# Kernel tuning notes

Hardware: AMD Instinct MI355X
Metric: run time of the kernel (lower is better)

The kernel has to match this reference:

```python
import jax, jax.numpy as jnp
import numpy as np

# Jamba mamba mixer dims
H = 4096      # hidden_size
D = 8192      # intermediate_size = mamba_expand * hidden_size
N = 16        # ssm_state_size (mamba_d_state)
K = 4         # conv_kernel_size (mamba_d_conv)
R = 256       # time_step_rank (mamba_dt_rank)
BATCH = 1
L = 2048
EPS = 1e-6


def setup_inputs() -> dict:
    key = jax.random.key(0)
    ks = jax.random.split(key, 10)
    s = 0.02
    return {
        "hidden_states": jax.random.normal(ks[0], (BATCH, L, H), jnp.float32),
        "W_in": jax.random.normal(ks[1], (2 * D, H), jnp.float32) * s,
        "conv_w": jax.random.normal(ks[2], (D, K), jnp.float32) * s,
        "conv_b": jax.random.normal(ks[3], (D,), jnp.float32) * s,
        "Wx": jax.random.normal(ks[4], (R + 2 * N, D), jnp.float32) * s,
        "dt_ln_w": jnp.ones((R,), jnp.float32),
        "b_ln_w": jnp.ones((N,), jnp.float32),
        "c_ln_w": jnp.ones((N,), jnp.float32),
        "Wdt": jax.random.normal(ks[5], (D, R), jnp.float32) * s,
        "dt_bias": jax.random.normal(ks[6], (D,), jnp.float32) * s,
        "A": -jnp.exp(jax.random.normal(ks[7], (D, N), jnp.float32) * 0.5),  # A = -exp(A_log)
        "D_param": jnp.ones((D,), jnp.float32),
        "W_out": jax.random.normal(ks[8], (H, D), jnp.float32) * s,
    }


def _rmsnorm(x, w):
    return x * jax.lax.rsqrt(jnp.mean(x * x, axis=-1, keepdims=True) + EPS) * w


def reference(hidden_states, W_in, conv_w, conv_b, Wx, dt_ln_w, b_ln_w, c_ln_w,
              Wdt, dt_bias, A, D_param, W_out):
    # in_proj -> [B, L, 2D]; split into ssm branch and gate
    proj = hidden_states @ W_in.T
    u, gate = jnp.split(proj, 2, axis=-1)

    # causal depthwise conv1d over sequence dim, then SiLU (causal_conv1d_fn)
    x = jnp.transpose(u, (0, 2, 1))  # [B, D, L]
    x = jax.lax.conv_general_dilated(
        x, conv_w[:, None, :], window_strides=(1,), padding=[(K - 1, 0)],
        dimension_numbers=("NCH", "OIH", "NCH"), feature_group_count=D)
    u = jax.nn.silu(jnp.transpose(x, (0, 2, 1)) + conv_b)  # [B, L, D]

    # x_proj -> dt / B / C with RMSNorms
    ssm_p = u @ Wx.T  # [B, L, R + 2N]
    dt, Bm, Cm = jnp.split(ssm_p, [R, R + N], axis=-1)
    dt = _rmsnorm(dt, dt_ln_w)
    Bm = _rmsnorm(Bm, b_ln_w)
    Cm = _rmsnorm(Cm, c_ln_w)

    # dt_proj (skip_bias_add: bias folded into softplus, delta_softplus=True)
    delta = jax.nn.softplus(dt @ Wdt.T + dt_bias)  # [B, L, D]

    # selective scan: state [B, D, N], recurrence over L
    def step(state, xs):
        d_t, B_t, C_t, u_t = xs  # [B,D], [B,N], [B,N], [B,D]
        dA = jnp.exp(d_t[..., None] * A)                       # [B, D, N]
        state = dA * state + (d_t * u_t)[..., None] * B_t[:, None, :]
        y_t = jnp.einsum("bdn,bn->bd", state, C_t)
        return state, y_t

    init = jnp.zeros((hidden_states.shape[0], D, N), hidden_states.dtype)
    xs = (jnp.swapaxes(delta, 0, 1), jnp.swapaxes(Bm, 0, 1),
          jnp.swapaxes(Cm, 0, 1), jnp.swapaxes(u, 0, 1))
    _, ys = jax.lax.scan(step, init, xs)  # ys: [L, B, D]

    y = jnp.swapaxes(ys, 0, 1) + u * D_param   # skip connection u * D
    y = y * jax.nn.silu(gate)                  # gated output
    return y @ W_out.T                         # out_proj -> [B, L, H]
```

## Files before the change

kernel.cpp:

```cpp
#include <hip/hip_runtime.h>
#include <stdint.h>


#define LSEQ 2048
#define HDIM 4096
#define DDIM 8192
#define NST  16
#define NPAD 384
#define NC   16
#define CLEN 128

typedef __bf16 bf16x8 __attribute__((ext_vector_type(8)));
typedef float  f32x4  __attribute__((ext_vector_type(4)));

__device__ __forceinline__ ushort f2b(float f) {
  uint32_t x = __float_as_uint(f);
  x += 0x7FFFu + ((x >> 16) & 1u);
  return (ushort)(x >> 16);
}
__device__ __forceinline__ float b2f(ushort u) {
  return __uint_as_float(((uint32_t)u) << 16);
}

__device__ __forceinline__ void gload_lds16(const ushort* g, ushort* l) {
  __builtin_amdgcn_global_load_lds(
      (const __attribute__((address_space(1))) void*)g,
      (__attribute__((address_space(3))) void*)l, 16, 0, 0);
}

__global__ __launch_bounds__(256) void cvt_kernel(const float* __restrict__ s,
                                                  ushort* __restrict__ d,
                                                  size_t n8) {
  size_t i = (size_t)blockIdx.x * 256 + threadIdx.x;
  if (i >= n8) return;
  const float4* sp = (const float4*)s;
  float4 a = sp[2 * i], b = sp[2 * i + 1];
  union { ushort us[8]; uint4 v; } u;
  u.us[0] = f2b(a.x); u.us[1] = f2b(a.y); u.us[2] = f2b(a.z); u.us[3] = f2b(a.w);
  u.us[4] = f2b(b.x); u.us[5] = f2b(b.y); u.us[6] = f2b(b.z); u.us[7] = f2b(b.w);
  ((uint4*)d)[i] = u.v;
}

template <int EPI>
__global__ __launch_bounds__(256) void gemm_nt(
    const ushort* __restrict__ A, const ushort* __restrict__ Bw,
    float* __restrict__ C, int M, int N, int ldk, int Kc,
    const float* __restrict__ bias) {
  __shared__ __align__(16) ushort As[128 * 64];
  __shared__ __align__(16) ushort Bs[128 * 64];
  const int tid  = threadIdx.x;
  const int lane = tid & 63;
  const int wid  = tid >> 6;
  const int wr = wid >> 1, wc = wid & 1;
  const int m0 = blockIdx.y * 128, n0 = blockIdx.x * 128;
  const int kbeg = blockIdx.z * Kc;
  C += (size_t)blockIdx.z * M * N;
  const int rr0 = tid >> 3;
  const int sl  = tid & 7;
  const int lrow = lane & 15;
  const int lks  = lane >> 4;

  f32x4 acc[4][4] = {};

  for (int k0 = kbeg; k0 < kbeg + Kc; k0 += 64) {
#pragma unroll
    for (int i = 0; i < 4; ++i) {
      int rr  = i * 32 + rr0;
      int ksl = sl ^ (rr & 7);
      const ushort* ga = A  + (size_t)(m0 + rr) * ldk + k0 + ksl * 8;
      const ushort* gb = Bw + (size_t)(n0 + rr) * ldk + k0 + ksl * 8;
      ushort* la = As + (i * 256 + (wid << 6)) * 8;
      ushort* lb = Bs + (i * 256 + (wid << 6)) * 8;
      gload_lds16(ga, la);
      gload_lds16(gb, lb);
    }
    __syncthreads();
#pragma unroll
    for (int kc = 0; kc < 2; ++kc) {
      bf16x8 av[4], bv[4];
#pragma unroll
      for (int mi = 0; mi < 4; ++mi) {
        int row = wr * 64 + mi * 16 + lrow;
        int ks  = kc * 4 + lks;
        av[mi] = *(const bf16x8*)(As + row * 64 + ((ks ^ (row & 7)) << 3));
      }
#pragma unroll
      for (int ni = 0; ni < 4; ++ni) {
        int row = wc * 64 + ni * 16 + lrow;
        int ks  = kc * 4 + lks;
        bv[ni] = *(const bf16x8*)(Bs + row * 64 + ((ks ^ (row & 7)) << 3));
      }
#pragma unroll
      for (int mi = 0; mi < 4; ++mi)
#pragma unroll
        for (int ni = 0; ni < 4; ++ni)
          acc[mi][ni] = __builtin_amdgcn_mfma_f32_16x16x32_bf16(
              av[mi], bv[ni], acc[mi][ni], 0, 0, 0);
    }
    __syncthreads();
  }

#pragma unroll
  for (int mi = 0; mi < 4; ++mi) {
    int row0 = m0 + wr * 64 + mi * 16 + (lks << 2);
#pragma unroll
    for (int ni = 0; ni < 4; ++ni) {
      int col = n0 + wc * 64 + ni * 16 + lrow;
      float bcol = 0.f;
      if (EPI == 1) bcol = bias[col];
#pragma unroll
      for (int q = 0; q < 4; ++q) {
        float v = acc[mi][ni][q];
        if (EPI == 1) {
          v += bcol;
          v = (v > 20.f) ? v : log1pf(__expf(v));
        }
        C[(size_t)(row0 + q) * N + col] = v;
      }
    }
  }
}

__global__ __launch_bounds__(256) void reduce8_kernel(
    const float* __restrict__ Cp, float* __restrict__ out) {
  size_t i = (size_t)blockIdx.x * 256 + threadIdx.x;
  const size_t MN = (size_t)LSEQ * NPAD;
  float s = 0.f;
#pragma unroll
  for (int z = 0; z < 8; ++z) s += Cp[z * MN + i];
  out[i] = s;
}

__global__ __launch_bounds__(256) void conv_silu_kernel(
    const float* __restrict__ ubuf, const float* __restrict__ cw,
    const float* __restrict__ cb, ushort* __restrict__ uc) {
  int d = blockIdx.x * 256 + threadIdx.x;
  int l = blockIdx.y;
  float4 w4 = ((const float4*)cw)[d];
  float wa[4] = {w4.x, w4.y, w4.z, w4.w};
  float s = cb[d];
#pragma unroll
  for (int j = 0; j < 4; ++j) {
    int li = l - 3 + j;
    if (li >= 0) s += wa[j] * ubuf[(size_t)li * DDIM + d];
  }
  float o = s / (1.f + __expf(-s));
  uc[(size_t)l * DDIM + d] = f2b(o);
}

__global__ __launch_bounds__(64) void norms_kernel(
    const float* __restrict__ ssmp, const float* __restrict__ dtw,
    const float* __restrict__ bw, const float* __restrict__ cwn,
    ushort* __restrict__ dtn, float* __restrict__ Bn, float* __restrict__ Cn) {
  int l = blockIdx.x, lane = threadIdx.x;
  const float* row = ssmp + (size_t)l * NPAD;
  float4 v = ((const float4*)row)[lane];
  float va[4] = {v.x, v.y, v.z, v.w};
  float ss = va[0]*va[0] + va[1]*va[1] + va[2]*va[2] + va[3]*va[3];
#pragma unroll
  for (int m = 32; m >= 1; m >>= 1) ss += __shfl_xor(ss, m);
  float rs = rsqrtf(ss * (1.f / 256.f) + 1e-6f);
  float4 w = ((const float4*)dtw)[lane];
  float wa[4] = {w.x, w.y, w.z, w.w};
  union { ushort us[4]; uint2 v2; } o;
#pragma unroll
  for (int j = 0; j < 4; ++j) o.us[j] = f2b(va[j] * rs * wa[j]);
  ((uint2*)(dtn + (size_t)l * 256))[lane] = o.v2;

  int g = lane & 15;
  float bv = row[256 + g], cv = row[272 + g];
  float bs = bv * bv, cs = cv * cv;
#pragma unroll
  for (int m = 8; m >= 1; m >>= 1) {
    bs += __shfl_xor(bs, m);
    cs += __shfl_xor(cs, m);
  }
  if (lane < 16) {
    Bn[(size_t)l * NST + lane] = bv * rsqrtf(bs * (1.f / 16.f) + 1e-6f) * bw[lane];
    Cn[(size_t)l * NST + lane] = cv * rsqrtf(cs * (1.f / 16.f) + 1e-6f) * cwn[lane];
  }
}


__global__ __launch_bounds__(256) void scan_phase1(
    const float* __restrict__ delta, const ushort* __restrict__ uc,
    const float* __restrict__ Bn, const float* __restrict__ Am,
    float* __restrict__ Sbuf, float* __restrict__ Pbuf) {
  __shared__ float sB[CLEN * NST];
  const int tid = threadIdx.x;
  const int d = blockIdx.x * 256 + tid;
  const int c = blockIdx.y, l0 = c * CLEN;
  {
    const float4* bsrc = (const float4*)(Bn + (size_t)l0 * NST);
    float4* bdst = (float4*)sB;
    for (int i = tid; i < CLEN * NST / 4; i += 256) bdst[i] = bsrc[i];
  }
  __syncthreads();
  float A[16];
#pragma unroll
  for (int j = 0; j < 4; ++j) {
    float4 a4 = ((const float4*)(Am + (size_t)d * NST))[j];
    A[4*j] = a4.x; A[4*j+1] = a4.y; A[4*j+2] = a4.z; A[4*j+3] = a4.w;
  }
  float st[16] = {};
  float sd = 0.f;
  const size_t base = (size_t)l0 * DDIM + d;
  float dx0 = delta[base],            dx1 = delta[base + DDIM];
  float ux0 = b2f(uc[base]),          ux1 = b2f(uc[base + DDIM]);
  for (int l = 0; l < CLEN; l += 2) {
    int lp = (l + 2 < CLEN) ? l + 2 : CLEN - 2;
    float dxn0 = delta[base + (size_t)lp * DDIM];
    float dxn1 = delta[base + (size_t)(lp + 1) * DDIM];
    float uxn0 = b2f(uc[base + (size_t)lp * DDIM]);
    float uxn1 = b2f(uc[base + (size_t)(lp + 1) * DDIM]);
    sd += dx0;
    float dxu = dx0 * ux0;
#pragma unroll
    for (int n = 0; n < 16; ++n)
      st[n] = fmaf(__expf(dx0 * A[n]), st[n], dxu * sB[l * NST + n]);
    sd += dx1;
    dxu = dx1 * ux1;
#pragma unroll
    for (int n = 0; n < 16; ++n)
      st[n] = fmaf(__expf(dx1 * A[n]), st[n], dxu * sB[(l + 1) * NST + n]);
    dx0 = dxn0; dx1 = dxn1; ux0 = uxn0; ux1 = uxn1;
  }
  float4* Sd = (float4*)(Sbuf + ((size_t)c * DDIM + d) * NST);
  float4* Pd = (float4*)(Pbuf + ((size_t)c * DDIM + d) * NST);
#pragma unroll
  for (int j = 0; j < 4; ++j) {
    Sd[j] = make_float4(st[4*j], st[4*j+1], st[4*j+2], st[4*j+3]);
    Pd[j] = make_float4(__expf(A[4*j] * sd),   __expf(A[4*j+1] * sd),
                        __expf(A[4*j+2] * sd), __expf(A[4*j+3] * sd));
  }
}

__global__ __launch_bounds__(256) void scan_phase2(
    const float* __restrict__ Sbuf, float* __restrict__ Pbuf) {
  size_t t = (size_t)blockIdx.x * 256 + threadIdx.x;
  const size_t stride = (size_t)DDIM * NST;
  float s = 0.f;
  for (int c = 0; c < NC; ++c) {
    float P = Pbuf[c * stride + t];
    float S = Sbuf[c * stride + t];
    Pbuf[c * stride + t] = s;
    s = fmaf(P, s, S);
  }
}

__global__ __launch_bounds__(256) void scan_phase3(
    const float* __restrict__ delta, const ushort* __restrict__ uc,
    const float* __restrict__ Bn, const float* __restrict__ Cn,
    const float* __restrict__ Am, const float* __restrict__ Ibuf,
    const float* __restrict__ gbuf, const float* __restrict__ Dp,
    ushort* __restrict__ yg) {
  __shared__ float sB[CLEN * NST];
  __shared__ float sC[CLEN * NST];
  const int tid = threadIdx.x;
  const int d = blockIdx.x * 256 + tid;
  const int c = blockIdx.y, l0 = c * CLEN;
  {
    const float4* bsrc = (const float4*)(Bn + (size_t)l0 * NST);
    const float4* csrc = (const float4*)(Cn + (size_t)l0 * NST);
    float4* bdst = (float4*)sB;
    float4* cdst = (float4*)sC;
    for (int i = tid; i < CLEN * NST / 4; i += 256) {
      bdst[i] = bsrc[i];
      cdst[i] = csrc[i];
    }
  }
  __syncthreads();
  float A[16], st[16];
#pragma unroll
  for (int j = 0; j < 4; ++j) {
    float4 a4 = ((const float4*)(Am + (size_t)d * NST))[j];
    A[4*j] = a4.x; A[4*j+1] = a4.y; A[4*j+2] = a4.z; A[4*j+3] = a4.w;
    float4 s4 = ((const float4*)(Ibuf + ((size_t)c * DDIM + d) * NST))[j];
    st[4*j] = s4.x; st[4*j+1] = s4.y; st[4*j+2] = s4.z; st[4*j+3] = s4.w;
  }
  const float Dpd = Dp[d];
  const size_t base = (size_t)l0 * DDIM + d;
  float dx0 = delta[base],   dx1 = delta[base + DDIM];
  float ux0 = b2f(uc[base]), ux1 = b2f(uc[base + DDIM]);
  float g0  = gbuf[base],    g1  = gbuf[base + DDIM];
  for (int l = 0; l < CLEN; l += 2) {
    int lp = (l + 2 < CLEN) ? l + 2 : CLEN - 2;
    float dxn0 = delta[base + (size_t)lp * DDIM];
    float dxn1 = delta[base + (size_t)(lp + 1) * DDIM];
    float uxn0 = b2f(uc[base + (size_t)lp * DDIM]);
    float uxn1 = b2f(uc[base + (size_t)(lp + 1) * DDIM]);
    float gn0  = gbuf[base + (size_t)lp * DDIM];
    float gn1  = gbuf[base + (size_t)(lp + 1) * DDIM];
    {
      float dxu = dx0 * ux0, y0 = 0.f, y1 = 0.f;
#pragma unroll
      for (int n = 0; n < 16; n += 2) {
        st[n]   = fmaf(__expf(dx0 * A[n]),   st[n],   dxu * sB[l * NST + n]);
        st[n+1] = fmaf(__expf(dx0 * A[n+1]), st[n+1], dxu * sB[l * NST + n+1]);
        y0 = fmaf(st[n],   sC[l * NST + n],   y0);
        y1 = fmaf(st[n+1], sC[l * NST + n+1], y1);
      }
      float o = (y0 + y1 + ux0 * Dpd) * (g0 / (1.f + __expf(-g0)));
      yg[base + (size_t)l * DDIM] = f2b(o);
    }
    {
      float dxu = dx1 * ux1, y0 = 0.f, y1 = 0.f;
#pragma unroll
      for (int n = 0; n < 16; n += 2) {
        st[n]   = fmaf(__expf(dx1 * A[n]),   st[n],   dxu * sB[(l+1) * NST + n]);
        st[n+1] = fmaf(__expf(dx1 * A[n+1]), st[n+1], dxu * sB[(l+1) * NST + n+1]);
        y0 = fmaf(st[n],   sC[(l+1) * NST + n],   y0);
        y1 = fmaf(st[n+1], sC[(l+1) * NST + n+1], y1);
      }
      float o = (y0 + y1 + ux1 * Dpd) * (g1 / (1.f + __expf(-g1)));
      yg[base + (size_t)(l + 1) * DDIM] = f2b(o);
    }
    dx0 = dxn0; dx1 = dxn1; ux0 = uxn0; ux1 = uxn1; g0 = gn0; g1 = gn1;
  }
}

extern "C" void kernel_launch(void* const* d_in, const int* in_sizes, int n_in,
                              void* d_out, int out_size, void* d_ws, size_t ws_size,
                              hipStream_t stream) {
  (void)in_sizes; (void)n_in; (void)out_size; (void)ws_size;
  const float* hs   = (const float*)d_in[0];
  const float* W_in = (const float*)d_in[1];
  const float* cw   = (const float*)d_in[2];
  const float* cb   = (const float*)d_in[3];
  const float* Wx   = (const float*)d_in[4];
  const float* dtw  = (const float*)d_in[5];
  const float* bw   = (const float*)d_in[6];
  const float* cwn  = (const float*)d_in[7];
  const float* Wdt  = (const float*)d_in[8];
  const float* dtb  = (const float*)d_in[9];
  const float* Am   = (const float*)d_in[10];
  const float* Dp   = (const float*)d_in[11];
  const float* Wout = (const float*)d_in[12];
  float* out = (float*)d_out;

  char* ws = (char*)d_ws;
  const size_t MB = 1ull << 20;
  ushort* win_b  = (ushort*)(ws);
  float*  delta  = (float*) (ws);
  ushort* wout_b = (ushort*)(ws + 64 * MB);
  float*  ubuf   = (float*) (ws + 128 * MB);
  float*  Cp     = (float*) (ws + 128 * MB);
  float*  Sbuf   = (float*) (ws + 152 * MB);
  float*  Pbuf   = (float*) (ws + 160 * MB);
  float*  gbuf   = (float*) (ws + 192 * MB);
  ushort* hs_b   = (ushort*)(ws + 256 * MB);
  ushort* wxp_b  = (ushort*)(ws + 272 * MB);
  ushort* wdt_b  = (ushort*)(ws + 278 * MB);
  ushort* ucv    = (ushort*)(ws + 282 * MB);
  float*  ssmp   = (float*) (ws + 314 * MB);
  ushort* dtn    = (ushort*)(ws + 317 * MB);
  float*  Bn     = (float*) (ws + 318 * MB);
  float*  Cn     = (float*) (ws + 318 * MB + 131072);
  ushort* yg     = (ushort*)(ws + 319 * MB);

  cvt_kernel<<<67108864 / 2048, 256, 0, stream>>>(W_in, win_b, 67108864 / 8);
  cvt_kernel<<<8388608 / 2048, 256, 0, stream>>>(hs, hs_b, 8388608 / 8);
  cvt_kernel<<<2359296 / 2048, 256, 0, stream>>>(Wx, wxp_b, 2359296 / 8);
  hipMemsetAsync((char*)wxp_b + 4718592, 0, 1572864, stream);
  cvt_kernel<<<2097152 / 2048, 256, 0, stream>>>(Wdt, wdt_b, 2097152 / 8);

  gemm_nt<0><<<dim3(64, 16), 256, 0, stream>>>(hs_b, win_b, ubuf,
                                               2048, DDIM, 4096, 4096, nullptr);
  gemm_nt<0><<<dim3(64, 16), 256, 0, stream>>>(hs_b, win_b + (size_t)DDIM * 4096,
                                               gbuf, 2048, DDIM, 4096, 4096, nullptr);
  cvt_kernel<<<33554432 / 2048, 256, 0, stream>>>(Wout, wout_b, 33554432 / 8);

  conv_silu_kernel<<<dim3(32, 2048), 256, 0, stream>>>(ubuf, cw, cb, ucv);

  gemm_nt<0><<<dim3(3, 16, 8), 256, 0, stream>>>(ucv, wxp_b, Cp,
                                                 2048, NPAD, 8192, 1024, nullptr);
  reduce8_kernel<<<3072, 256, 0, stream>>>(Cp, ssmp);

  norms_kernel<<<2048, 64, 0, stream>>>(ssmp, dtw, bw, cwn, dtn, Bn, Cn);

  gemm_nt<1><<<dim3(64, 16), 256, 0, stream>>>(dtn, wdt_b, delta,
                                               2048, DDIM, 256, 256, dtb);

  scan_phase1<<<dim3(32, NC), 256, 0, stream>>>(delta, ucv, Bn, Am, Sbuf, Pbuf);
  scan_phase2<<<512, 256, 0, stream>>>(Sbuf, Pbuf);
  scan_phase3<<<dim3(32, NC), 256, 0, stream>>>(delta, ucv, Bn, Cn, Am, Pbuf,
                                                gbuf, Dp, yg);

  gemm_nt<0><<<dim3(32, 16), 256, 0, stream>>>(yg, wout_b, out,
                                               2048, 4096, 8192, 8192, nullptr);
}
```

Before: 962.9 us.

## Add 256x256 8-wave pipelined GEMM with swizzle and split-K out_proj

Adds a new 512-thread GEMM kernel with 256x256 tiles, double-buffered LDS filled through direct global-to-LDS loads, XOR-swizzled LDS layout, interleaved load/MFMA phases with setprio, and an XCD-aware block swizzle. It replaces the two in_proj GEMMs and the out_proj GEMM. The out_proj is split-K by 2 and followed by a reduction kernel, to fill more CUs with the larger tiles. The cost is 128 KB of LDS per block and an extra fp32 partial write and read for out_proj.

```diff
diff --git a/kernel.cpp b/kernel.cpp
--- a/kernel.cpp
+++ b/kernel.cpp
@@ -39,6 +39,128 @@
   u.us[0] = f2b(a.x); u.us[1] = f2b(a.y); u.us[2] = f2b(a.z); u.us[3] = f2b(a.w);
   u.us[4] = f2b(b.x); u.us[5] = f2b(b.y); u.us[6] = f2b(b.z); u.us[7] = f2b(b.w);
   ((uint4*)d)[i] = u.v;
+}
+
+__global__ __launch_bounds__(512, 2) void gemm8p(
+    const ushort* __restrict__ A, const ushort* __restrict__ Bw,
+    float* __restrict__ C, int M, int N, int ldk, int Kc) {
+  __shared__ __align__(16) ushort As[2][256 * 64];
+  __shared__ __align__(16) ushort Bs[2][256 * 64];
+  const int tid  = threadIdx.x;
+  const int lane = tid & 63;
+  const int w    = tid >> 6;
+  const int wr   = w >> 2;
+  const int wc   = w & 3;
+
+  const int nbx = gridDim.x;
+  const int nwg = nbx * gridDim.y;
+  int bid = blockIdx.y * nbx + blockIdx.x;
+  const int cpx = nwg >> 3;
+  int swz = (bid & 7) * cpx + (bid >> 3);
+  const int m0 = (swz / nbx) * 256, n0 = (swz % nbx) * 256;
+  const int kbeg = blockIdx.z * Kc;
+  C += (size_t)blockIdx.z * M * N;
+  const int NT = Kc >> 6;
+
+  const int srck = (lane & 7) ^ ((lane >> 3) & 7);
+  const int astripe = w >> 2, awl = w & 3;
+  const int arow_st = astripe * 128 + awl * 8 + (lane >> 3);
+  const ushort* Abase = A + (size_t)(m0 + arow_st) * ldk + kbeg + srck * 8;
+  const int aldsb = (astripe * 128 + awl * 8) * 64;
+  const int brow_st = w * 8 + (lane >> 3);
+  const ushort* Bbase = Bw + (size_t)(n0 + brow_st) * ldk + kbeg + srck * 8;
+  const int bldsb = (w * 8) * 64;
+
+  const int lrow = lane & 15;
+  const int kch  = lane >> 4;
+  const int axor = lrow & 7;
+
+  auto stA = [&](int buf, int kt, int q) {
+    gload_lds16(Abase + (size_t)q * 32 * ldk + kt * 64,
+                &As[buf][aldsb + q * 32 * 64]);
+  };
+  auto stB = [&](int buf, int kt, int half, int j) {
+    gload_lds16(Bbase + (size_t)(half * 128 + j * 64) * ldk + kt * 64,
+                &Bs[buf][bldsb + (half * 128 + j * 64) * 64]);
+  };
+  auto rdA = [&](int buf, int mi, int sl) -> bf16x8 {
+    int arow = wr * 128 + mi * 16 + lrow;
+    int s4 = sl * 4 + kch;
+    return *(const bf16x8*)&As[buf][arow * 64 + ((s4 ^ axor) << 3)];
+  };
+  auto rdB = [&](int buf, int ni, int sl) -> bf16x8 {
+    int brow = wc * 64 + ni * 16 + lrow;
+    int s4 = sl * 4 + kch;
+    return *(const bf16x8*)&Bs[buf][brow * 64 + ((s4 ^ axor) << 3)];
+  };
+
+  f32x4 acc[8][4] = {};
+
+  stB(0, 0, 0, 0); stB(0, 0, 0, 1); stB(0, 0, 1, 0); stB(0, 0, 1, 1);
+  stA(0, 0, 0); stA(0, 0, 1); stA(0, 0, 2); stA(0, 0, 3);
+  stB(1, 1, 0, 0); stB(1, 1, 0, 1); stB(1, 1, 1, 0); stB(1, 1, 1, 1);
+  stA(1, 1, 0); stA(1, 1, 1);
+  asm volatile("s_waitcnt vmcnt(6)" ::: "memory");
+  asm volatile("s_barrier" ::: "memory");
+
+#define PHASE(BUF, Q, STAGES)                                                 \
+  {                                                                           \
+    if (Q == 0) {                                                             \
+      _Pragma("unroll") for (int ni = 0; ni < 4; ++ni)                        \
+        _Pragma("unroll") for (int sl = 0; sl < 2; ++sl)                      \
+          bfr[ni][sl] = rdB(BUF, ni, sl);                                     \
+    }                                                                         \
+    _Pragma("unroll") for (int m2 = 0; m2 < 2; ++m2)                          \
+      _Pragma("unroll") for (int sl = 0; sl < 2; ++sl)                        \
+        afr[m2][sl] = rdA(BUF, Q * 2 + m2, sl);                               \
+    STAGES;                                                                   \
+    asm volatile("s_barrier" ::: "memory");                                   \
+    __builtin_amdgcn_s_setprio(1);                                            \
+    _Pragma("unroll") for (int sl = 0; sl < 2; ++sl)                          \
+      _Pragma("unroll") for (int m2 = 0; m2 < 2; ++m2)                        \
+        _Pragma("unroll") for (int ni = 0; ni < 4; ++ni)                      \
+          acc[Q * 2 + m2][ni] = __builtin_amdgcn_mfma_f32_16x16x32_bf16(      \
+              afr[m2][sl], bfr[ni][sl], acc[Q * 2 + m2][ni], 0, 0, 0);        \
+    __builtin_amdgcn_s_setprio(0);                                            \
+  }
+
+  for (int t = 0; t < NT; t += 2) {
+    const int t2 = (t + 2 < NT) ? t + 2 : 0;
+    const int t3 = (t + 3 < NT) ? t + 3 : 0;
+    bf16x8 bfr[4][2], afr[2][2];
+    PHASE(0, 0, { stA(1, t + 1, 2); stA(1, t + 1, 3); });
+    asm volatile("s_barrier" ::: "memory");
+    PHASE(0, 1, { stB(0, t2, 0, 0); stB(0, t2, 0, 1); });
+    asm volatile("s_barrier" ::: "memory");
+    PHASE(0, 2, { stB(0, t2, 1, 0); stB(0, t2, 1, 1); });
+    asm volatile("s_barrier" ::: "memory");
+    PHASE(0, 3, { stA(0, t2, 0); stA(0, t2, 1); });
+    asm volatile("s_waitcnt vmcnt(6)" ::: "memory");
+    asm volatile("s_barrier" ::: "memory");
+    PHASE(1, 0, { stA(0, t2, 2); stA(0, t2, 3); });
+    asm volatile("s_barrier" ::: "memory");
+    PHASE(1, 1, { stB(1, t3, 0, 0); stB(1, t3, 0, 1); });
+    asm volatile("s_barrier" ::: "memory");
+    PHASE(1, 2, { stB(1, t3, 1, 0); stB(1, t3, 1, 1); });
+    asm volatile("s_barrier" ::: "memory");
+    PHASE(1, 3, { stA(1, t3, 0); stA(1, t3, 1); });
+    asm volatile("s_waitcnt vmcnt(6)" ::: "memory");
+    asm volatile("s_barrier" ::: "memory");
+  }
+#undef PHASE
+
+  asm volatile("s_waitcnt vmcnt(0)" ::: "memory");
+#pragma unroll
+  for (int mi = 0; mi < 8; ++mi) {
+    int row0 = m0 + wr * 128 + mi * 16 + kch * 4;
+#pragma unroll
+    for (int ni = 0; ni < 4; ++ni) {
+      int col = n0 + wc * 64 + ni * 16 + lrow;
+#pragma unroll
+      for (int q_ = 0; q_ < 4; ++q_)
+        C[(size_t)(row0 + q_) * N + col] = acc[mi][ni][q_];
+    }
+  }
 }
 
 template <int EPI>
@@ -131,6 +253,15 @@
   out[i] = s;
 }
 
+__global__ __launch_bounds__(256) void reduce2_kernel(
+    const float* __restrict__ Cp, float* __restrict__ out) {
+  size_t i = (size_t)blockIdx.x * 256 + threadIdx.x;
+  const size_t MN4 = (size_t)LSEQ * HDIM / 4;
+  float4 a = ((const float4*)Cp)[i];
+  float4 b = ((const float4*)Cp)[MN4 + i];
+  ((float4*)out)[i] = make_float4(a.x + b.x, a.y + b.y, a.z + b.z, a.w + b.w);
+}
+
 __global__ __launch_bounds__(256) void conv_silu_kernel(
     const float* __restrict__ ubuf, const float* __restrict__ cw,
     const float* __restrict__ cb, ushort* __restrict__ uc) {
@@ -180,7 +311,6 @@
     Cn[(size_t)l * NST + lane] = cv * rsqrtf(cs * (1.f / 16.f) + 1e-6f) * cwn[lane];
   }
 }
-
 
 __global__ __launch_bounds__(256) void scan_phase1(
     const float* __restrict__ delta, const ushort* __restrict__ uc,
@@ -345,6 +475,7 @@
   ushort* wout_b = (ushort*)(ws + 64 * MB);
   float*  ubuf   = (float*) (ws + 128 * MB);
   float*  Cp     = (float*) (ws + 128 * MB);
+  float*  Cp2    = (float*) (ws + 128 * MB);
   float*  Sbuf   = (float*) (ws + 152 * MB);
   float*  Pbuf   = (float*) (ws + 160 * MB);
   float*  gbuf   = (float*) (ws + 192 * MB);
@@ -364,10 +495,10 @@
   hipMemsetAsync((char*)wxp_b + 4718592, 0, 1572864, stream);
   cvt_kernel<<<2097152 / 2048, 256, 0, stream>>>(Wdt, wdt_b, 2097152 / 8);
 
-  gemm_nt<0><<<dim3(64, 16), 256, 0, stream>>>(hs_b, win_b, ubuf,
-                                               2048, DDIM, 4096, 4096, nullptr);
-  gemm_nt<0><<<dim3(64, 16), 256, 0, stream>>>(hs_b, win_b + (size_t)DDIM * 4096,
-                                               gbuf, 2048, DDIM, 4096, 4096, nullptr);
+  gemm8p<<<dim3(32, 8), 512, 0, stream>>>(hs_b, win_b, ubuf,
+                                          2048, DDIM, 4096, 4096);
+  gemm8p<<<dim3(32, 8), 512, 0, stream>>>(hs_b, win_b + (size_t)DDIM * 4096,
+                                          gbuf, 2048, DDIM, 4096, 4096);
   cvt_kernel<<<33554432 / 2048, 256, 0, stream>>>(Wout, wout_b, 33554432 / 8);
 
   conv_silu_kernel<<<dim3(32, 2048), 256, 0, stream>>>(ubuf, cw, cb, ucv);
@@ -386,6 +517,7 @@
   scan_phase3<<<dim3(32, NC), 256, 0, stream>>>(delta, ucv, Bn, Cn, Am, Pbuf,
                                                 gbuf, Dp, yg);
 
-  gemm_nt<0><<<dim3(32, 16), 256, 0, stream>>>(yg, wout_b, out,
-                                               2048, 4096, 8192, 8192, nullptr);
-}
+  gemm8p<<<dim3(16, 8, 2), 512, 0, stream>>>(yg, wout_b, Cp2,
+                                             2048, HDIM, 8192, 4096);
+  reduce2_kernel<<<(LSEQ * HDIM / 4) / 256, 256, 0, stream>>>(Cp2, out);
+}
```

Result: faster. 893.2 us (-7.2%).
